# Kernel tuning notes

Hardware: AMD Instinct MI355X
Metric: run time of the kernel (lower is better)

Reference implementation:

```python
import jax, jax.numpy as jnp
import numpy as np

K = 3          # kernel size
STRIDE = 1
PAD = 1
DIL = 1
K2 = K * K     # number of sampling locations per output pixel


def conv2d(x, w, b, stride=STRIDE, pad=PAD, dil=DIL):
    # x: [B,C,H,W], w: [O,I,K,K], b: [O]
    out = jax.lax.conv_general_dilated(
        x, w, window_strides=(stride, stride),
        padding=[(pad, pad), (pad, pad)], rhs_dilation=(dil, dil),
        dimension_numbers=('NCHW', 'OIHW', 'NCHW'))
    return out + b[None, :, None, None]


def bilinear_sample(x, sy, sx):
    # x: [B,C,H,W]; sy, sx: [B,K2,Ho,Wo] float sampling coords (y, x)
    # zero padding outside the image (torchvision deform_conv2d semantics)
    B, C, H, W = x.shape
    x_flat = x.reshape(B, C, H * W)

    y0 = jnp.floor(sy)
    x0 = jnp.floor(sx)
    wy1 = sy - y0  # frac weights
    wx1 = sx - x0
    wy0 = 1.0 - wy1
    wx0 = 1.0 - wx1

    def gather(yi, xi):
        valid = ((yi >= 0) & (yi < H) & (xi >= 0) & (xi < W)).astype(x.dtype)
        yc = jnp.clip(yi, 0, H - 1).astype(jnp.int32)
        xc = jnp.clip(xi, 0, W - 1).astype(jnp.int32)
        idx = (yc * W + xc).reshape(B, 1, -1)  # [B,1,K2*Ho*Wo]
        v = jnp.take_along_axis(x_flat, idx, axis=2)  # [B,C,K2*Ho*Wo]
        v = v.reshape(B, C, *yi.shape[1:])            # [B,C,K2,Ho,Wo]
        return v * valid[:, None]

    out = (gather(y0,     x0    ) * (wy0 * wx0)[:, None]
         + gather(y0,     x0 + 1) * (wy0 * wx1)[:, None]
         + gather(y0 + 1, x0    ) * (wy1 * wx0)[:, None]
         + gather(y0 + 1, x0 + 1) * (wy1 * wx1)[:, None])
    return out  # [B,C,K2,Ho,Wo]


def setup_inputs() -> dict:
    key = jax.random.key(0)
    ks = jax.random.split(key, 6)
    B, C, H, W = 4, 64, 128, 128
    Cout = 64
    x = jax.random.normal(ks[0], (B, C, H, W), jnp.float32)
    # offset conv: 2*K2 output channels; small init -> small offsets (realistic)
    w_off = jax.random.normal(ks[1], (2 * K2, C, K, K), jnp.float32) * 0.01
    b_off = jnp.zeros((2 * K2,), jnp.float32)
    # mask conv: K2 output channels, sigmoid activation
    w_mask = jax.random.normal(ks[2], (K2, C, K, K), jnp.float32) * 0.01
    b_mask = jnp.zeros((K2,), jnp.float32)  # mask_init_bias = 0
    # main deformable conv weights
    w = jax.random.normal(ks[3], (Cout, C, K, K), jnp.float32) * (1.0 / np.sqrt(C * K2))
    b = jnp.zeros((Cout,), jnp.float32)
    return {"x": x, "w_off": w_off, "b_off": b_off,
            "w_mask": w_mask, "b_mask": b_mask, "w": w, "b": b}


def reference(x, w_off, b_off, w_mask, b_mask, w, b):
    B, C, H, W = x.shape
    Cout = w.shape[0]

    offset = conv2d(x, w_off, b_off)                    # [B,2*K2,Ho,Wo]
    mask = jax.nn.sigmoid(conv2d(x, w_mask, b_mask))    # [B,K2,Ho,Wo]
    Ho, Wo = offset.shape[2], offset.shape[3]

    off = offset.reshape(B, K2, 2, Ho, Wo)
    dy, dx = off[:, :, 0], off[:, :, 1]                 # torchvision layout: (y,x) pairs

    ki = (jnp.arange(K2) // K).astype(jnp.float32)      # kernel row index
    kj = (jnp.arange(K2) % K).astype(jnp.float32)       # kernel col index
    base_y = (jnp.arange(Ho, dtype=jnp.float32) * STRIDE - PAD)[None, :, None] \
             + (ki * DIL)[:, None, None]                # [K2,Ho,1]
    base_x = (jnp.arange(Wo, dtype=jnp.float32) * STRIDE - PAD)[None, None, :] \
             + (kj * DIL)[:, None, None]                # [K2,1,Wo]

    sy = base_y[None] + dy                              # [B,K2,Ho,Wo]
    sx = base_x[None] + dx

    sampled = bilinear_sample(x, sy, sx) * mask[:, None]  # [B,C,K2,Ho,Wo]
    out = jnp.einsum('bckhw,ock->bohw', sampled, w.reshape(Cout, C, K2))
    return out + b[None, :, None, None]
```

## Files before the change

### kernel.cpp

```cpp
#include <hip/hip_runtime.h>
#include <math.h>

typedef __attribute__((ext_vector_type(8))) short short8;
typedef __attribute__((ext_vector_type(4))) float f32x4;
typedef unsigned short ushort_t;
typedef unsigned int uint_t;

#define HH 128
#define WW 128
#define CC 64
#define HWp 16384

__device__ inline ushort_t f2bf(float f) {
    uint_t u = __float_as_uint(f);
    uint_t r = (u + 0x7FFFu + ((u >> 16) & 1u)) >> 16;
    return (ushort_t)r;
}
__device__ inline float blo(uint_t u) { return __uint_as_float(u << 16); }
__device__ inline float bhi(uint_t u) { return __uint_as_float(u & 0xFFFF0000u); }
__device__ inline short8 bc8(uint4 v) { return __builtin_bit_cast(short8, v); }

__device__ inline uint_t pk2(f32x4 wv, uint_t a, uint_t b, uint_t c, uint_t d) {
    float lo = wv.x * blo(a) + wv.y * blo(b) + wv.z * blo(c) + wv.w * blo(d);
    float hi = wv.x * bhi(a) + wv.y * bhi(b) + wv.z * bhi(c) + wv.w * bhi(d);
    uint_t r;
    asm("v_cvt_pk_bf16_f32 %0, %1, %2" : "=v"(r) : "v"(lo), "v"(hi));
    return r;
}
__device__ inline short8 bilerp8(f32x4 wv, uint4 A, uint4 B, uint4 C, uint4 D) {
    uint4 r;
    r.x = pk2(wv, A.x, B.x, C.x, D.x);
    r.y = pk2(wv, A.y, B.y, C.y, D.y);
    r.z = pk2(wv, A.z, B.z, C.z, D.z);
    r.w = pk2(wv, A.w, B.w, C.w, D.w);
    return __builtin_bit_cast(short8, r);
}

__global__ __launch_bounds__(256) void k_prep(const float* __restrict__ x,
        ushort_t* __restrict__ xtb,
        const float* __restrict__ w_off, const float* __restrict__ w_mask,
        const float* __restrict__ w,
        ushort_t* __restrict__ wpom, ushort_t* __restrict__ wpm) {
    __shared__ __align__(16) float tile[64][68];
    int bid = blockIdx.x;
    int t = threadIdx.x;
    if (bid < 1024) {
        int xs = (bid & 1) * 64;
        int y  = (bid >> 1) & 127;
        int b  = bid >> 8;
#pragma unroll
        for (int i = 0; i < 4; ++i) {
            int c  = i * 16 + (t >> 4);
            int xl = (t & 15) << 2;
            float4 v = *(const float4*)&x[(((size_t)b * CC + c) * HH + y) * WW + xs + xl];
            *(float4*)&tile[c][xl] = v;
        }
        __syncthreads();
#pragma unroll
        for (int i = 0; i < 8; ++i) {
            int pxl = i * 8 + (t >> 5);
            int cp  = t & 31;
            float v0 = tile[cp * 2][pxl], v1 = tile[cp * 2 + 1][pxl];
            uint_t pk;
            asm("v_cvt_pk_bf16_f32 %0, %1, %2" : "=v"(pk) : "v"(v0), "v"(v1));
            *(uint_t*)&xtb[(((size_t)b * HH + y) * WW + xs + pxl) * CC + cp * 2] = pk;
        }
    } else {
        int idx = (bid - 1024) * 256 + t;
        if (idx < 18432) {
            int e = idx;
            int j = e & 7, l = (e >> 3) & 63, mf = (e >> 9) & 1, ks = e >> 10;
            int ch = mf * 16 + (l & 15);
            int k = ks * 32 + ((l >> 4) << 3) + j;
            int c = k & 63, kk = k >> 6;
            float v = 0.f;
            if (ch < 18) v = w_off[(ch * CC + c) * 9 + kk];
            else if (ch < 27) v = w_mask[((ch - 18) * CC + c) * 9 + kk];
            wpom[idx] = f2bf(v);
        } else if (idx < 18432 + 36864) {
            int e = idx - 18432;
            int j = e & 7, l = (e >> 3) & 63, mf = (e >> 9) & 3, ks = e >> 11;
            int o = mf * 16 + (l & 15);
            int k = ks * 32 + ((l >> 4) << 3) + j;
            int c = k & 63, kk = k >> 6;
            wpm[e] = f2bf(w[(o * CC + c) * 9 + kk]);
        }
    }
}

__global__ __launch_bounds__(256, 6) void k_conv_om(const ushort_t* __restrict__ xtb,
        const uint4* __restrict__ wpom, const float* __restrict__ b_off,
        const float* __restrict__ b_mask, float* __restrict__ om) {
    __shared__ ushort_t xrow[3 * 68 * 64];
    int blk = blockIdx.x;
    int b = blk >> 8, rem = blk & 255;
    int y = rem >> 1, xh = (rem & 1) * 64;
    int t = threadIdx.x;

    for (int ky = 0; ky < 3; ++ky) {
        int yy = y + ky - 1;
        bool rok = (yy >= 0) && (yy < HH);
#pragma unroll
        for (int i = 0; i < 3; ++i) {
            int t2 = i * 256 + t;
            if (t2 < 528) {
                int cl = t2 >> 3;
                int c0 = (t2 & 7) * 8;
                int xcoord = xh - 1 + cl;
                bool ok = rok && (xcoord >= 0) && (xcoord < WW);
                uint4 v = make_uint4(0u, 0u, 0u, 0u);
                if (ok) v = *(const uint4*)&xtb[(((size_t)b * HWp) + yy * WW + xcoord) * CC + c0];
                int idx = ((ky * 68 + cl) * 64 + c0) ^ ((cl & 7) << 3);
                *(uint4*)&xrow[idx] = v;
            }
        }
    }
    __syncthreads();

    int lane = t & 63, w = t >> 6;
    int lm = lane & 15, lg = lane >> 4;
    int pxl = w * 16 + lm;
    f32x4 acc[2] = {};
#pragma unroll
    for (int ks = 0; ks < 18; ++ks) {
        int kk = ks >> 1;
        int kyy = kk / 3, kxx = kk % 3;
        int c0 = (ks & 1) * 32 + lg * 8;
        short8 a0 = bc8(wpom[(ks * 2 + 0) * 64 + lane]);
        short8 a1 = bc8(wpom[(ks * 2 + 1) * 64 + lane]);
        int cl = pxl + kxx;
        int idx = ((kyy * 68 + cl) * 64 + c0) ^ ((cl & 7) << 3);
        short8 bf = *(const short8*)&xrow[idx];
        acc[0] = __builtin_amdgcn_mfma_f32_16x16x32_bf16(a0, bf, acc[0], 0, 0, 0);
        acc[1] = __builtin_amdgcn_mfma_f32_16x16x32_bf16(a1, bf, acc[1], 0, 0, 0);
    }
    int xg = (xh >> 4) + w;
    size_t tb = ((size_t)((b * 128 + y) * 8 + xg)) * 432;
#pragma unroll
    for (int mf = 0; mf < 2; ++mf)
#pragma unroll
        for (int r = 0; r < 4; ++r) {
            int ch = mf * 16 + lg * 4 + r;
            if (ch < 27) {
                float v = acc[mf][r] + (ch < 18 ? b_off[ch] : b_mask[ch - 18]);
                if (ch >= 18) v = 1.f / (1.f + __expf(-v));
                om[tb + ch * 16 + lm] = v;
            }
        }
}

__global__ __launch_bounds__(256, 8) void k_fused(const ushort_t* __restrict__ xtb,
        const float* __restrict__ omt, const uint4* __restrict__ wpm,
        const float* __restrict__ bias, float* __restrict__ out) {
    __shared__ __align__(16) ushort_t sm[16 * 576];
    int blk = blockIdx.x;
    int b = blk >> 10, rem = blk & 1023;
    int y = rem >> 3, xg = rem & 7, xs = xg << 4;
    int t = threadIdx.x, lane = t & 63, w = t >> 6;
    const char* xbB = (const char*)xtb + ((size_t)b << 21);
    const float* omb = omt + ((size_t)((b * 128 + y) * 8 + xg)) * 432;

    float pw0 = 0.f, pw1 = 0.f, pw2 = 0.f, pw3 = 0.f;
    int paT = 0, paB = 0, ppk = 0;
    if (lane < 36) {
        int pxl = lane / 9, k = lane - pxl * 9;
        int px_t = (w << 2) + pxl;
        int ki = k / 3, kj = k - ki * 3;
        int x = xs + px_t;
        float dy = omb[32 * k + px_t];
        float dx = omb[32 * k + 16 + px_t];
        float m  = omb[288 + 16 * k + px_t];
        float sy = (float)(y - 1 + ki) + dy;
        float sx = (float)(x - 1 + kj) + dx;
        float fy = floorf(sy), fx = floorf(sx);
        float wy1 = sy - fy, wx1 = sx - fx;
        float wy0 = 1.f - wy1, wx0 = 1.f - wx1;
        int iy0 = (int)fy, ix0 = (int)fx;
        int iy1 = iy0 + 1, ix1 = ix0 + 1;
        bool vy0 = (iy0 >= 0) & (iy0 < HH);
        bool vy1 = (iy1 >= 0) & (iy1 < HH);
        float wyr0 = vy0 ? wy0 : (vy1 ? wy1 : 0.f);
        int   ry0  = vy0 ? iy0 : (vy1 ? iy1 : 0);
        float wyr1 = (vy0 & vy1) ? wy1 : 0.f;
        int   ry1  = min(max(iy1, 0), HH - 1);
        int bx = min(max(ix0, 0), WW - 2);
        float wxh0 = (bx == ix0) ? wx0 : ((bx == ix1) ? wx1 : 0.f);
        float wxh1 = (bx + 1 == ix1) ? wx1 : ((bx + 1 == ix0) ? wx0 : 0.f);
        pw0 = m * wyr0 * wxh0;
        pw1 = m * wyr0 * wxh1;
        pw2 = m * wyr1 * wxh0;
        pw3 = m * wyr1 * wxh1;
        paT = (int)((uint_t)(((ry0 << 7) + bx) << 7));
        paB = (int)((uint_t)(((ry1 << 7) + bx) << 7));
        ppk = (int)((uint_t)(px_t * 576 + k * 64) |
                    ((uint_t)(((px_t ^ k) & 7) << 3) << 16));
    }

    {
        int g = lane >> 3, j = lane & 7;
        uint_t j16 = (uint_t)(j << 4);
        uint_t jw  = (uint_t)(j << 3);
        int slA = g;
        float wA0 = __shfl(pw0, slA), wA1 = __shfl(pw1, slA);
        float wA2 = __shfl(pw2, slA), wA3 = __shfl(pw3, slA);
        uint_t aTA = (uint_t)__shfl(paT, slA) + j16;
        uint_t aBA = (uint_t)__shfl(paB, slA) + j16;
        uint_t pkA = (uint_t)__shfl(ppk, slA);
        uint4 tlA = *(const uint4*)(xbB + aTA);
        uint4 trA = *(const uint4*)(xbB + aTA + 128);
        uint4 blA = *(const uint4*)(xbB + aBA);
        uint4 brA = *(const uint4*)(xbB + aBA + 128);
#pragma unroll
        for (int r = 0; r < 5; ++r) {
            float wB0, wB1, wB2, wB3;
            uint_t pkB = 0;
            uint4 tlB, trB, blB, brB;
            if (r < 4) {
                int slB = g + (r + 1) * 8; slB = slB > 35 ? 35 : slB;
                wB0 = __shfl(pw0, slB); wB1 = __shfl(pw1, slB);
                wB2 = __shfl(pw2, slB); wB3 = __shfl(pw3, slB);
                uint_t aTB = (uint_t)__shfl(paT, slB) + j16;
                uint_t aBB = (uint_t)__shfl(paB, slB) + j16;
                pkB = (uint_t)__shfl(ppk, slB);
                tlB = *(const uint4*)(xbB + aTB);
                trB = *(const uint4*)(xbB + aTB + 128);
                blB = *(const uint4*)(xbB + aBB);
                brB = *(const uint4*)(xbB + aBB + 128);
            }
            f32x4 wv = { wA0, wA1, wA2, wA3 };
            short8 bf = bilerp8(wv, tlA, trA, blA, brA);
            if (r < 4 || g < 4) {
                uint_t widx = ((pkA & 0xFFFFu) + jw) ^ (pkA >> 16);
                *(short8*)&sm[widx] = bf;
            }
            wA0 = wB0; wA1 = wB1; wA2 = wB2; wA3 = wB3;
            pkA = pkB;
            tlA = tlB; trA = trB; blA = blB; brA = brB;
        }
    }
    __syncthreads();

    int lm = lane & 15, lg = lane >> 4;
    f32x4 acc = {};
#pragma unroll
    for (int ks = 0; ks < 18; ++ks) {
        short8 af = bc8(wpm[((ks << 2) + w) * 64 + lane]);
        int bidx = (lm * 576 + (ks << 5) + (lg << 3)) ^ (((lm ^ (ks >> 1)) & 7) << 3);
        short8 bf = *(const short8*)&sm[bidx];
        acc = __builtin_amdgcn_mfma_f32_16x16x32_bf16(af, bf, acc, 0, 0, 0);
    }
#pragma unroll
    for (int r = 0; r < 4; ++r) {
        int o = (w << 4) + (lg << 2) + r;
        out[(((size_t)b * 64 + o) << 14) + (y << 7) + xs + lm] = acc[r] + bias[o];
    }
}

extern "C" void kernel_launch(void* const* d_in, const int* in_sizes, int n_in,
                              void* d_out, int out_size, void* d_ws, size_t ws_size,
                              hipStream_t stream) {
    const float* x      = (const float*)d_in[0];
    const float* w_off  = (const float*)d_in[1];
    const float* b_off  = (const float*)d_in[2];
    const float* w_mask = (const float*)d_in[3];
    const float* b_mask = (const float*)d_in[4];
    const float* w      = (const float*)d_in[5];
    const float* bias   = (const float*)d_in[6];
    float* out = (float*)d_out;

    char* ws = (char*)d_ws;
    ushort_t* xtb  = (ushort_t*)(ws);
    float*    om   = (float*)(ws + 8388608);
    ushort_t* wpom = (ushort_t*)(ws + 15466496);
    ushort_t* wpm  = (ushort_t*)(ws + 15503360);

    hipLaunchKernelGGL(k_prep, dim3(1240), dim3(256), 0, stream,
                       x, xtb, w_off, w_mask, w, wpom, wpm);
    hipLaunchKernelGGL(k_conv_om, dim3(1024), dim3(256), 0, stream,
                       xtb, (const uint4*)wpom, b_off, b_mask, om);
    hipLaunchKernelGGL(k_fused, dim3(4096), dim3(256), 0, stream,
                       xtb, om, (const uint4*)wpm, bias, out);
}
```

Baseline: 49.15 us.

## Merge offset/mask conv into the transpose kernel, reading fp32 input directly

Weight packing moves into its own small kernel. The x-to-bf16 NHWC transpose and the offset/mask convolution now run as two block ranges of a single launch. The conv blocks load fp32 x straight from NCHW and convert to bf16 in shared memory instead of waiting for the transposed buffer, which removes the dependency on the transpose and lets both block ranges run concurrently. In exchange the x rows are read twice (once by the transpose, once by the conv), the conv-side loads are scalar fp32 rather than vector loads, and conv blocks read packed weights from a k_pack launch that must finish first.

```diff
diff --git a/kernel.cpp b/kernel.cpp
--- a/kernel.cpp
+++ b/kernel.cpp
@@ -36,15 +36,40 @@
     return __builtin_bit_cast(short8, r);
 }
 
-__global__ __launch_bounds__(256) void k_prep(const float* __restrict__ x,
-        ushort_t* __restrict__ xtb,
-        const float* __restrict__ w_off, const float* __restrict__ w_mask,
-        const float* __restrict__ w,
+__global__ __launch_bounds__(256) void k_pack(const float* __restrict__ w_off,
+        const float* __restrict__ w_mask, const float* __restrict__ w,
         ushort_t* __restrict__ wpom, ushort_t* __restrict__ wpm) {
-    __shared__ __align__(16) float tile[64][68];
+    int idx = blockIdx.x * 256 + threadIdx.x;
+    if (idx < 18432) {
+        int e = idx;
+        int j = e & 7, l = (e >> 3) & 63, mf = (e >> 9) & 1, ks = e >> 10;
+        int ch = mf * 16 + (l & 15);
+        int k = ks * 32 + ((l >> 4) << 3) + j;
+        int c = k & 63, kk = k >> 6;
+        float v = 0.f;
+        if (ch < 18) v = w_off[(ch * CC + c) * 9 + kk];
+        else if (ch < 27) v = w_mask[((ch - 18) * CC + c) * 9 + kk];
+        wpom[idx] = f2bf(v);
+    } else if (idx < 18432 + 36864) {
+        int e = idx - 18432;
+        int j = e & 7, l = (e >> 3) & 63, mf = (e >> 9) & 3, ks = e >> 11;
+        int o = mf * 16 + (l & 15);
+        int k = ks * 32 + ((l >> 4) << 3) + j;
+        int c = k & 63, kk = k >> 6;
+        wpm[e] = f2bf(w[(o * CC + c) * 9 + kk]);
+    }
+}
+
+__global__ __launch_bounds__(256, 6) void k_stage(const float* __restrict__ x,
+        ushort_t* __restrict__ xtb, const uint4* __restrict__ wpom,
+        const float* __restrict__ b_off, const float* __restrict__ b_mask,
+        float* __restrict__ om) {
+    __shared__ __align__(16) char ldsbuf[3 * 68 * 64 * 2];
     int bid = blockIdx.x;
     int t = threadIdx.x;
+
     if (bid < 1024) {
+        float (*tile)[68] = (float (*)[68])ldsbuf;
         int xs = (bid & 1) * 64;
         int y  = (bid >> 1) & 127;
         int b  = bid >> 8;
@@ -65,59 +90,53 @@
             asm("v_cvt_pk_bf16_f32 %0, %1, %2" : "=v"(pk) : "v"(v0), "v"(v1));
             *(uint_t*)&xtb[(((size_t)b * HH + y) * WW + xs + pxl) * CC + cp * 2] = pk;
         }
-    } else {
-        int idx = (bid - 1024) * 256 + t;
-        if (idx < 18432) {
-            int e = idx;
-            int j = e & 7, l = (e >> 3) & 63, mf = (e >> 9) & 1, ks = e >> 10;
-            int ch = mf * 16 + (l & 15);
-            int k = ks * 32 + ((l >> 4) << 3) + j;
-            int c = k & 63, kk = k >> 6;
-            float v = 0.f;
-            if (ch < 18) v = w_off[(ch * CC + c) * 9 + kk];
-            else if (ch < 27) v = w_mask[((ch - 18) * CC + c) * 9 + kk];
-            wpom[idx] = f2bf(v);
-        } else if (idx < 18432 + 36864) {
-            int e = idx - 18432;
-            int j = e & 7, l = (e >> 3) & 63, mf = (e >> 9) & 3, ks = e >> 11;
-            int o = mf * 16 + (l & 15);
-            int k = ks * 32 + ((l >> 4) << 3) + j;
-            int c = k & 63, kk = k >> 6;
-            wpm[e] = f2bf(w[(o * CC + c) * 9 + kk]);
-        }
-    }
-}
-
-__global__ __launch_bounds__(256, 6) void k_conv_om(const ushort_t* __restrict__ xtb,
-        const uint4* __restrict__ wpom, const float* __restrict__ b_off,
-        const float* __restrict__ b_mask, float* __restrict__ om) {
-    __shared__ ushort_t xrow[3 * 68 * 64];
-    int blk = blockIdx.x;
-    int b = blk >> 8, rem = blk & 255;
-    int y = rem >> 1, xh = (rem & 1) * 64;
-    int t = threadIdx.x;
-
-    for (int ky = 0; ky < 3; ++ky) {
+        return;
+    }
+
+    ushort_t* xrow = (ushort_t*)ldsbuf;
+    int rem = bid - 1024;
+    int b = rem >> 8;
+    int y = (rem >> 1) & 127;
+    int xh = (rem & 1) * 64;
+    int lane = t & 63, w = t >> 6;
+
+#pragma unroll
+    for (int r = 0; r < 24; ++r) {
+        int ky = r >> 3;
+        int cp = (w << 3) + (r & 7);
         int yy = y + ky - 1;
         bool rok = (yy >= 0) && (yy < HH);
-#pragma unroll
-        for (int i = 0; i < 3; ++i) {
-            int t2 = i * 256 + t;
-            if (t2 < 528) {
-                int cl = t2 >> 3;
-                int c0 = (t2 & 7) * 8;
-                int xcoord = xh - 1 + cl;
-                bool ok = rok && (xcoord >= 0) && (xcoord < WW);
-                uint4 v = make_uint4(0u, 0u, 0u, 0u);
-                if (ok) v = *(const uint4*)&xtb[(((size_t)b * HWp) + yy * WW + xcoord) * CC + c0];
-                int idx = ((ky * 68 + cl) * 64 + c0) ^ ((cl & 7) << 3);
-                *(uint4*)&xrow[idx] = v;
-            }
-        }
+        float v0 = 0.f, v1 = 0.f;
+        if (rok) {
+            size_t base = ((size_t)(b * CC + cp * 2) * HH + yy) * WW + xh + lane;
+            v0 = x[base];
+            v1 = x[base + (size_t)HWp];
+        }
+        uint_t pk;
+        asm("v_cvt_pk_bf16_f32 %0, %1, %2" : "=v"(pk) : "v"(v0), "v"(v1));
+        int cl = lane + 1;
+        int idx = ((ky * 68 + cl) * 64 + cp * 2) ^ ((cl & 7) << 3);
+        *(uint_t*)&xrow[idx] = pk;
+    }
+    if (t < 192) {
+        int ky = t >> 6, rr = t & 63, cp = rr >> 1, side = rr & 1;
+        int yy = y + ky - 1;
+        int xcoord = side ? xh + 64 : xh - 1;
+        bool ok = (yy >= 0) && (yy < HH) && (xcoord >= 0) && (xcoord < WW);
+        float v0 = 0.f, v1 = 0.f;
+        if (ok) {
+            size_t base = ((size_t)(b * CC + cp * 2) * HH + yy) * WW + xcoord;
+            v0 = x[base];
+            v1 = x[base + (size_t)HWp];
+        }
+        uint_t pk;
+        asm("v_cvt_pk_bf16_f32 %0, %1, %2" : "=v"(pk) : "v"(v0), "v"(v1));
+        int cl = side ? 65 : 0;
+        int idx = ((ky * 68 + cl) * 64 + cp * 2) ^ ((cl & 7) << 3);
+        *(uint_t*)&xrow[idx] = pk;
     }
     __syncthreads();
 
-    int lane = t & 63, w = t >> 6;
     int lm = lane & 15, lg = lane >> 4;
     int pxl = w * 16 + lm;
     f32x4 acc[2] = {};
@@ -274,10 +293,10 @@
     ushort_t* wpom = (ushort_t*)(ws + 15466496);
     ushort_t* wpm  = (ushort_t*)(ws + 15503360);
 
-    hipLaunchKernelGGL(k_prep, dim3(1240), dim3(256), 0, stream,
-                       x, xtb, w_off, w_mask, w, wpom, wpm);
-    hipLaunchKernelGGL(k_conv_om, dim3(1024), dim3(256), 0, stream,
-                       xtb, (const uint4*)wpom, b_off, b_mask, om);
+    hipLaunchKernelGGL(k_pack, dim3(216), dim3(256), 0, stream,
+                       w_off, w_mask, w, wpom, wpm);
+    hipLaunchKernelGGL(k_stage, dim3(2048), dim3(256), 0, stream,
+                       x, xtb, (const uint4*)wpom, b_off, b_mask, om);
     hipLaunchKernelGGL(k_fused, dim3(4096), dim3(256), 0, stream,
                        xtb, om, (const uint4*)wpm, bias, out);
 }
```

Measured after the change: 57.76 us. 1.18x slower.
